# Kernel tuning notes

Measured on AMD Instinct MI355X. Metric: run time of the kernel, lower is better.

The kernel has to match this reference:

```python
import jax, jax.numpy as jnp
import numpy as np

B, S, D, E, K = 4, 2048, 1024, 8, 2
EPS, W_THRES, TEMP = 1e-4, 0.1, 1.0


def setup_inputs() -> dict:
    key = jax.random.key(0)
    k1, k2, k3, k4, k5 = jax.random.split(key, 5)
    x = jax.random.normal(k1, (B, S, D), dtype=jnp.float32)
    gate_W = jax.random.normal(k2, (D, E), dtype=jnp.float32) * 0.02
    gate_b = jnp.zeros((E,), dtype=jnp.float32)
    expert_W = jax.random.normal(k3, (E, D, D), dtype=jnp.float32) * 0.02
    expert_b = jnp.zeros((E, D), dtype=jnp.float32)
    return {"x": x, "gate_W": gate_W, "gate_b": gate_b,
            "expert_W": expert_W, "expert_b": expert_b}


def reference(x, gate_W, gate_b, expert_W, expert_b):
    # Gating: linear -> temperature -> clamp-min(eps) -> softmax
    scores = jnp.maximum((x @ gate_W + gate_b) / TEMP, EPS)      # [B,S,E]
    p = jax.nn.softmax(scores, axis=-1)                           # [B,S,E]
    _, topk_idx = jax.lax.top_k(p, K)                             # [B,S,K]
    # boolean membership mask of selected experts
    topk_mask = jax.nn.one_hot(topk_idx, E, dtype=p.dtype).sum(-2) > 0  # [B,S,E]
    # weights: clamp-min(weight_thres), normalized by detached sum over selected
    w = jnp.maximum(p, W_THRES)                                   # [B,S,E]
    w_gather = jnp.take_along_axis(w, topk_idx, axis=-1)          # [B,S,K]
    total = jax.lax.stop_gradient(w_gather.sum(-1, keepdims=True))
    w = w / total
    comb = jnp.where(topk_mask, w, jnp.zeros_like(w))             # [B,S,E]
    # Dense equivalent of gather/expert/scatter loop (E small): each expert
    # is Linear(D, D); masked combine weights zero out unselected experts.
    y = jnp.einsum('bsd,edf->bsef', x, expert_W) + expert_b       # [B,S,E,D]
    out = jnp.einsum('bsef,bse->bsf', y, comb) / K                # [B,S,D]
    return out
```

## Files before the change

kernel.cpp:

```cpp
#include <hip/hip_runtime.h>
#include <hip/hip_fp16.h>
#include <stdint.h>

#define TOK 8192
#define DIM 1024
#define NE 8
#define NTILE 136

typedef short bf16x8 __attribute__((ext_vector_type(8)));
typedef float f32x4 __attribute__((ext_vector_type(4)));

__device__ __forceinline__ unsigned short f2bf(float f) {
  unsigned int u = __float_as_uint(f);
  u += 0x7FFFu + ((u >> 16) & 1u);
  return (unsigned short)(u >> 16);
}

__device__ __forceinline__ void gl_lds16(const void* g, void* l) {
  __builtin_amdgcn_global_load_lds(
      (__attribute__((address_space(1))) unsigned int*)(g),
      (__attribute__((address_space(3))) unsigned int*)(l), 16, 0, 0);
}

__global__ __launch_bounds__(256) void gate_kernel(
    const float* __restrict__ x, const float* __restrict__ gW,
    const float* __restrict__ gb, unsigned short* __restrict__ xb,
    int* __restrict__ eSel, float* __restrict__ wSel, int* __restrict__ cnt)
{
  if (blockIdx.x == 0 && threadIdx.x < NE) cnt[threadIdx.x] = 0;

  __shared__ float gWs[NE * DIM];
#pragma unroll
  for (int h = 0; h < 8; ++h) {
    const int m = threadIdx.x + h * 256;
    float4 v = ((const float4*)gW)[m];
    const int d = m >> 1, e0 = (m & 1) * 4;
    gWs[(e0 + 0) * DIM + d] = v.x;
    gWs[(e0 + 1) * DIM + d] = v.y;
    gWs[(e0 + 2) * DIM + d] = v.z;
    gWs[(e0 + 3) * DIM + d] = v.w;
  }
  __syncthreads();

  const int wave = threadIdx.x >> 6;
  const int lane = threadIdx.x & 63;
  const int t = blockIdx.x * 4 + wave;
  const float4* xrow = (const float4*)(x + (size_t)t * DIM);
  ushort4* xbrow = (ushort4*)(xb + (size_t)t * DIM);

  double acc[NE];
#pragma unroll
  for (int e = 0; e < NE; ++e) acc[e] = 0.0;

#pragma unroll
  for (int i = 0; i < 4; ++i) {
    const int j = i * 64 + lane;
    float4 v = xrow[j];
    ushort4 pk;
    pk.x = f2bf(v.x); pk.y = f2bf(v.y); pk.z = f2bf(v.z); pk.w = f2bf(v.w);
    xbrow[j] = pk;
#pragma unroll
    for (int e = 0; e < NE; ++e) {
      float4 gv = *(const float4*)&gWs[e * DIM + j * 4];
      acc[e] += (double)v.x * (double)gv.x + (double)v.y * (double)gv.y
              + (double)v.z * (double)gv.z + (double)v.w * (double)gv.w;
    }
  }
#pragma unroll
  for (int off = 32; off > 0; off >>= 1) {
#pragma unroll
    for (int e = 0; e < NE; ++e)
      acc[e] += __shfl_xor(acc[e], off, 64);
  }

  if (lane == 0) {
    double s[NE];
#pragma unroll
    for (int e = 0; e < NE; ++e) {
      s[e] = acc[e] + (double)gb[e];
      if (s[e] < 1e-4) s[e] = 1e-4;
    }
    int e0 = 0;
    for (int e = 1; e < NE; ++e) if (s[e] > s[e0]) e0 = e;
    int e1 = (e0 == 0) ? 1 : 0;
    for (int e = 0; e < NE; ++e) if (e != e0 && s[e] > s[e1]) e1 = e;
    float m = (float)s[e0];
    float Z = 0.f, pf[NE];
#pragma unroll
    for (int e = 0; e < NE; ++e) { pf[e] = __expf((float)s[e] - m); Z += pf[e]; }
    float w0 = pf[e0] / Z; if (w0 < 0.1f) w0 = 0.1f;
    float w1 = pf[e1] / Z; if (w1 < 0.1f) w1 = 0.1f;
    const float inv = 0.5f / (w0 + w1);
    eSel[t * 2 + 0] = e0;
    eSel[t * 2 + 1] = e1;
    wSel[t * 2 + 0] = w0 * inv;
    wSel[t * 2 + 1] = w1 * inv;
  }
}

__global__ __launch_bounds__(256) void scatter_kernel(
    const int* __restrict__ eSel, const float* __restrict__ wSel,
    int* __restrict__ cnt, int* __restrict__ listTok, float* __restrict__ listW)
{
  __shared__ int lcnt[NE];
  __shared__ int base[NE];
  const int tid = threadIdx.x;
  if (tid < NE) lcnt[tid] = 0;
  __syncthreads();

  const int t = blockIdx.x * 256 + tid;
  const int e0 = eSel[t * 2 + 0];
  const int e1 = eSel[t * 2 + 1];
  const float w0 = wSel[t * 2 + 0];
  const float w1 = wSel[t * 2 + 1];
  const int l0 = atomicAdd(&lcnt[e0], 1);
  const int l1 = atomicAdd(&lcnt[e1], 1);
  __syncthreads();
  if (tid < NE) base[tid] = atomicAdd(&cnt[tid], lcnt[tid]);
  __syncthreads();

  const int p0 = base[e0] + l0;
  listTok[e0 * TOK + p0] = t * 2 + 0;
  listW [e0 * TOK + p0] = w0;
  const int p1 = base[e1] + l1;
  listTok[e1 * TOK + p1] = t * 2 + 1;
  listW [e1 * TOK + p1] = w1;
}

__global__ __launch_bounds__(256) void transpose_w(
    const float* __restrict__ W, unsigned short* __restrict__ Wt)
{
  __shared__ float t2[64][65];
  const int b  = blockIdx.x;
  const int e  = b >> 8;
  const int db = (b >> 4) & 15;
  const int fb = b & 15;
  const int d0 = db * 64, f0 = fb * 64;
  const int tid = threadIdx.x;
#pragma unroll
  for (int h = 0; h < 4; ++h) {
    const int idx = tid + h * 256;
    const int r = idx >> 4, c4 = idx & 15;
    float4 v = *(const float4*)&W[((size_t)e * DIM + d0 + r) * DIM + f0 + c4 * 4];
    t2[r][c4 * 4 + 0] = v.x;
    t2[r][c4 * 4 + 1] = v.y;
    t2[r][c4 * 4 + 2] = v.z;
    t2[r][c4 * 4 + 3] = v.w;
  }
  __syncthreads();
#pragma unroll
  for (int h = 0; h < 8; ++h) {
    const int o = tid + h * 256;
    const int f = o >> 5, k2 = (o & 31) * 2;
    const unsigned int lo = f2bf(t2[k2][f]);
    const unsigned int hi = f2bf(t2[k2 + 1][f]);
    *(unsigned int*)&Wt[((size_t)e * DIM + f0 + f) * DIM + d0 + k2] =
        lo | (hi << 16);
  }
}

__global__ __launch_bounds__(256) void moe_gemm(
    const unsigned short* __restrict__ xb, const unsigned short* __restrict__ Wt,
    const float* __restrict__ eb, const int* __restrict__ cnt,
    const int* __restrict__ listTok, const float* __restrict__ listW,
    __half* __restrict__ yslot)
{
  const int dId = blockIdx.x % NTILE;
  const int cT  = blockIdx.x / NTILE;
  int e = -1, r0 = 0, rows = 0, accT = 0;
#pragma unroll
  for (int ee = 0; ee < NE; ++ee) {
    const int c = cnt[ee];
    const int nt = (c + 127) >> 7;
    if (dId >= accT && dId < accT + nt) {
      e = ee; r0 = (dId - accT) * 128;
      rows = c - r0; if (rows > 128) rows = 128;
    }
    accT += nt;
  }
  if (e < 0) return;

  __shared__ __align__(16) unsigned short As[4][128 * 32];
  __shared__ __align__(16) unsigned short Bs[4][128 * 32];
  __shared__ int   tid_s[128];
  __shared__ float w_s[128];

  const int tid = threadIdx.x;
  if (tid < 128) {
    if (tid < rows) {
      tid_s[tid] = listTok[e * TOK + r0 + tid];
      w_s[tid]   = listW [e * TOK + r0 + tid];
    } else {
      tid_s[tid] = 0;
      w_s[tid]   = 0.0f;
    }
  }
  __syncthreads();

  const int w    = tid >> 6;
  const int lane = tid & 63;
  const int qsrc = (lane & 3) ^ ((lane >> 3) & 3);
  const int rA0  = w * 32 + (lane >> 2);
  const int rA1  = rA0 + 16;
  const unsigned short* srcA0 = xb + (size_t)(tid_s[rA0] >> 1) * DIM + qsrc * 8;
  const unsigned short* srcA1 = xb + (size_t)(tid_s[rA1] >> 1) * DIM + qsrc * 8;
  const unsigned short* srcB0 = Wt + ((size_t)e * DIM + cT * 128 + rA0) * DIM + qsrc * 8;
  const unsigned short* srcB1 = Wt + ((size_t)e * DIM + cT * 128 + rA1) * DIM + qsrc * 8;

  const int wr = w >> 1, wc = w & 1;
  const int mrow = lane & 15;
  const int qg   = lane >> 4;
  const int qsA  = (qg ^ ((mrow >> 1) & 3)) * 8;

  f32x4 acc[4][4];
#pragma unroll
  for (int i = 0; i < 4; ++i)
#pragma unroll
    for (int j = 0; j < 4; ++j)
      acc[i][j] = {0.f, 0.f, 0.f, 0.f};

#pragma unroll
  for (int p = 0; p < 3; ++p) {
    unsigned short* a = &As[p][w * 1024];
    unsigned short* b = &Bs[p][w * 1024];
    gl_lds16(srcA0 + p * 32, a);
    gl_lds16(srcA1 + p * 32, a + 512);
    gl_lds16(srcB0 + p * 32, b);
    gl_lds16(srcB1 + p * 32, b + 512);
  }
  asm volatile("s_waitcnt vmcnt(8)" ::: "memory");
  __builtin_amdgcn_s_barrier();

  for (int kc = 0; kc < DIM / 32; ++kc) {
    const int cur = kc & 3;
    if (kc + 3 < DIM / 32) {
      const int k1 = (kc + 3) * 32;
      const int nb = (kc + 3) & 3;
      unsigned short* a = &As[nb][w * 1024];
      unsigned short* b = &Bs[nb][w * 1024];
      gl_lds16(srcA0 + k1, a);
      gl_lds16(srcA1 + k1, a + 512);
      gl_lds16(srcB0 + k1, b);
      gl_lds16(srcB1 + k1, b + 512);
    }
    bf16x8 af[4], bfr[4];
#pragma unroll
    for (int mt = 0; mt < 4; ++mt)
      af[mt] = *(const bf16x8*)&As[cur][(wr * 64 + mt * 16 + mrow) * 32 + qsA];
#pragma unroll
    for (int nt = 0; nt < 4; ++nt)
      bfr[nt] = *(const bf16x8*)&Bs[cur][(wc * 64 + nt * 16 + mrow) * 32 + qsA];
#pragma unroll
    for (int mt = 0; mt < 4; ++mt)
#pragma unroll
      for (int nt = 0; nt < 4; ++nt)
        acc[mt][nt] = __builtin_amdgcn_mfma_f32_16x16x32_bf16(
            af[mt], bfr[nt], acc[mt][nt], 0, 0, 0);
    if (kc < DIM / 32 - 1) {
      if (kc < DIM / 32 - 3)
        asm volatile("s_waitcnt vmcnt(8) lgkmcnt(0)" ::: "memory");
      else if (kc == DIM / 32 - 3)
        asm volatile("s_waitcnt vmcnt(4) lgkmcnt(0)" ::: "memory");
      else
        asm volatile("s_waitcnt vmcnt(0) lgkmcnt(0)" ::: "memory");
      __builtin_amdgcn_s_barrier();
    }
  }

  const int colBase = cT * 128 + wc * 64 + mrow;
  float bias[4];
#pragma unroll
  for (int nt = 0; nt < 4; ++nt)
    bias[nt] = eb[(size_t)e * DIM + colBase + nt * 16];
#pragma unroll
  for (int mt = 0; mt < 4; ++mt) {
#pragma unroll
    for (int r = 0; r < 4; ++r) {
      const int rloc = wr * 64 + mt * 16 + (lane >> 4) * 4 + r;
      if (rloc < rows) {
        const int tk    = tid_s[rloc];
        const float wgt = w_s[rloc];
        __half* dst = yslot + ((size_t)(tk & 1) * TOK + (size_t)(tk >> 1)) * DIM;
#pragma unroll
        for (int nt = 0; nt < 4; ++nt)
          dst[colBase + nt * 16] = __float2half(wgt * (acc[mt][nt][r] + bias[nt]));
      }
    }
  }
}

__global__ __launch_bounds__(256) void combine(
    const __half* __restrict__ y0, const __half* __restrict__ y1,
    float4* __restrict__ out)
{
  const size_t i = (size_t)blockIdx.x * 256 + threadIdx.x;
  const ushort4 ua = ((const ushort4*)y0)[i];
  const ushort4 ub = ((const ushort4*)y1)[i];
  const __half* ah = (const __half*)&ua;
  const __half* bh = (const __half*)&ub;
  float4 o;
  o.x = __half2float(ah[0]) + __half2float(bh[0]);
  o.y = __half2float(ah[1]) + __half2float(bh[1]);
  o.z = __half2float(ah[2]) + __half2float(bh[2]);
  o.w = __half2float(ah[3]) + __half2float(bh[3]);
  out[i] = o;
}

extern "C" void kernel_launch(void* const* d_in, const int* in_sizes, int n_in,
                              void* d_out, int out_size, void* d_ws, size_t ws_size,
                              hipStream_t stream)
{
  const float* x  = (const float*)d_in[0];
  const float* gW = (const float*)d_in[1];
  const float* gb = (const float*)d_in[2];
  const float* eW = (const float*)d_in[3];
  const float* eb = (const float*)d_in[4];
  float* out = (float*)d_out;

  char* p = (char*)d_ws;
  unsigned short* xb = (unsigned short*)p;  p += (size_t)TOK * DIM * 2;
  unsigned short* Wt = (unsigned short*)p;  p += (size_t)NE * DIM * DIM * 2;
  __half* yslot = (__half*)p;               p += (size_t)2 * TOK * DIM * 2;
  int* cnt = (int*)p;                       p += 256;
  int* listTok = (int*)p;                   p += (size_t)NE * TOK * 4;
  float* listW = (float*)p;                 p += (size_t)NE * TOK * 4;

  int*   eSel = (int*)yslot;
  float* wSel = (float*)((char*)yslot + TOK * 8);

  gate_kernel<<<TOK / 4, 256, 0, stream>>>(x, gW, gb, xb, eSel, wSel, cnt);
  scatter_kernel<<<TOK / 256, 256, 0, stream>>>(eSel, wSel, cnt, listTok, listW);
  transpose_w<<<NE * 256, 256, 0, stream>>>(eW, Wt);
  moe_gemm<<<NTILE * 8, 256, 0, stream>>>(xb, Wt, eb, cnt, listTok, listW, yslot);
  combine<<<TOK * DIM / 4 / 256, 256, 0, stream>>>(
      yslot, yslot + (size_t)TOK * DIM, (float4*)out);
}
```

Measured before the change: 214.1 us.

## Widen MoE GEMM tile to 128x256 with 512 threads and phased pipeline

The expert GEMM block goes from 256 threads computing a 128x128 tile to 512 threads computing a 128x256 tile. The grid drops from 8 to 4 column tiles per row tile, and each token row of A is loaded once per 256 output columns, halving A re-reads. The K loop is restructured into half-chunk phases with a 3-stage LDS ring, a barrier between LDS reads and MFMA, and s_setprio raised around the MFMA block, with an explicit vmcnt wait schedule. This raises LDS use and halves the number of blocks, which risks lower occupancy and less parallelism for the small-expert tiles.

Result: faster. 208.3 us (-2.7%).

```diff
diff --git a/kernel.cpp b/kernel.cpp
--- a/kernel.cpp
+++ b/kernel.cpp
@@ -6,6 +6,7 @@
 #define DIM 1024
 #define NE 8
 #define NTILE 136
+#define NCT 4
 
 typedef short bf16x8 __attribute__((ext_vector_type(8)));
 typedef float f32x4 __attribute__((ext_vector_type(4)));
@@ -159,7 +160,40 @@
   }
 }
 
-__global__ __launch_bounds__(256) void moe_gemm(
+#define WAITVM(n) asm volatile("s_waitcnt vmcnt(" #n ")" ::: "memory")
+
+#define STG3(t, h, stb)                                                      \
+  { const int off_ = (t) * 64 + (h) * 32;                                    \
+    unsigned short* Ad_ = (unsigned short*)As + ((stb) * 2 + (h)) * (128 * 32) + w * 512;  \
+    unsigned short* Bd_ = (unsigned short*)Bs + ((stb) * 2 + (h)) * (256 * 32) + w * 1024; \
+    gl_lds16(srcA  + off_, Ad_);                                             \
+    gl_lds16(srcB0 + off_, Bd_);                                             \
+    gl_lds16(srcB1 + off_, Bd_ + 512); }
+
+#define PHASE(t, h, bufv, stb, DO_STAGE, VMA)                                \
+  { const unsigned short* Ab_ = (const unsigned short*)As + ((bufv) * 2 + (h)) * (128 * 32); \
+    const unsigned short* Bb_ = (const unsigned short*)Bs + ((bufv) * 2 + (h)) * (256 * 32); \
+    bf16x8 af[4], bfr[4];                                                    \
+    _Pragma("unroll")                                                        \
+    for (int mt = 0; mt < 4; ++mt)                                           \
+      af[mt] = *(const bf16x8*)&Ab_[(wr * 64 + mt * 16 + mrow) * 32 + sA];   \
+    _Pragma("unroll")                                                        \
+    for (int nt = 0; nt < 4; ++nt)                                           \
+      bfr[nt] = *(const bf16x8*)&Bb_[(wc * 64 + nt * 16 + mrow) * 32 + sA];  \
+    if (DO_STAGE) { STG3((t) + 2, h, stb); }                                 \
+    __builtin_amdgcn_s_barrier();                                            \
+    __builtin_amdgcn_s_setprio(1);                                           \
+    _Pragma("unroll")                                                        \
+    for (int mt = 0; mt < 4; ++mt)                                           \
+      _Pragma("unroll")                                                      \
+      for (int nt = 0; nt < 4; ++nt)                                         \
+        acc[mt][nt] = __builtin_amdgcn_mfma_f32_16x16x32_bf16(               \
+            af[mt], bfr[nt], acc[mt][nt], 0, 0, 0);                          \
+    __builtin_amdgcn_s_setprio(0);                                           \
+    VMA;                                                                     \
+    __builtin_amdgcn_s_barrier(); }
+
+__global__ __launch_bounds__(512, 2) void moe_gemm(
     const unsigned short* __restrict__ xb, const unsigned short* __restrict__ Wt,
     const float* __restrict__ eb, const int* __restrict__ cnt,
     const int* __restrict__ listTok, const float* __restrict__ listW,
@@ -180,8 +214,8 @@
   }
   if (e < 0) return;
 
-  __shared__ __align__(16) unsigned short As[4][128 * 32];
-  __shared__ __align__(16) unsigned short Bs[4][128 * 32];
+  __shared__ __align__(16) unsigned short As[3 * 2 * 128 * 32];
+  __shared__ __align__(16) unsigned short Bs[3 * 2 * 256 * 32];
   __shared__ int   tid_s[128];
   __shared__ float w_s[128];
 
@@ -199,18 +233,19 @@
 
   const int w    = tid >> 6;
   const int lane = tid & 63;
-  const int qsrc = (lane & 3) ^ ((lane >> 3) & 3);
-  const int rA0  = w * 32 + (lane >> 2);
-  const int rA1  = rA0 + 16;
-  const unsigned short* srcA0 = xb + (size_t)(tid_s[rA0] >> 1) * DIM + qsrc * 8;
-  const unsigned short* srcA1 = xb + (size_t)(tid_s[rA1] >> 1) * DIM + qsrc * 8;
-  const unsigned short* srcB0 = Wt + ((size_t)e * DIM + cT * 128 + rA0) * DIM + qsrc * 8;
-  const unsigned short* srcB1 = Wt + ((size_t)e * DIM + cT * 128 + rA1) * DIM + qsrc * 8;
-
-  const int wr = w >> 1, wc = w & 1;
+  const int rA  = w * 16 + (lane >> 2);
+  const int qA  = (lane & 3) ^ (rA & 3);
+  const unsigned short* srcA = xb + (size_t)(tid_s[rA] >> 1) * DIM + qA * 8;
+  const int rB0 = w * 32 + (lane >> 2);
+  const int rB1 = rB0 + 16;
+  const int qB  = (lane & 3) ^ (rB0 & 3);
+  const unsigned short* srcB0 = Wt + ((size_t)e * DIM + cT * 256 + rB0) * DIM + qB * 8;
+  const unsigned short* srcB1 = Wt + ((size_t)e * DIM + cT * 256 + rB1) * DIM + qB * 8;
+
+  const int wr = w >> 2, wc = w & 3;
   const int mrow = lane & 15;
   const int qg   = lane >> 4;
-  const int qsA  = (qg ^ ((mrow >> 1) & 3)) * 8;
+  const int sA   = (qg ^ (mrow & 3)) * 8;
 
   f32x4 acc[4][4];
 #pragma unroll
@@ -219,55 +254,24 @@
     for (int j = 0; j < 4; ++j)
       acc[i][j] = {0.f, 0.f, 0.f, 0.f};
 
-#pragma unroll
-  for (int p = 0; p < 3; ++p) {
-    unsigned short* a = &As[p][w * 1024];
-    unsigned short* b = &Bs[p][w * 1024];
-    gl_lds16(srcA0 + p * 32, a);
-    gl_lds16(srcA1 + p * 32, a + 512);
-    gl_lds16(srcB0 + p * 32, b);
-    gl_lds16(srcB1 + p * 32, b + 512);
-  }
-  asm volatile("s_waitcnt vmcnt(8)" ::: "memory");
+  STG3(0, 0, 0); STG3(0, 1, 0); STG3(1, 0, 1); STG3(1, 1, 1);
+  WAITVM(9);
   __builtin_amdgcn_s_barrier();
 
-  for (int kc = 0; kc < DIM / 32; ++kc) {
-    const int cur = kc & 3;
-    if (kc + 3 < DIM / 32) {
-      const int k1 = (kc + 3) * 32;
-      const int nb = (kc + 3) & 3;
-      unsigned short* a = &As[nb][w * 1024];
-      unsigned short* b = &Bs[nb][w * 1024];
-      gl_lds16(srcA0 + k1, a);
-      gl_lds16(srcA1 + k1, a + 512);
-      gl_lds16(srcB0 + k1, b);
-      gl_lds16(srcB1 + k1, b + 512);
-    }
-    bf16x8 af[4], bfr[4];
-#pragma unroll
-    for (int mt = 0; mt < 4; ++mt)
-      af[mt] = *(const bf16x8*)&As[cur][(wr * 64 + mt * 16 + mrow) * 32 + qsA];
-#pragma unroll
-    for (int nt = 0; nt < 4; ++nt)
-      bfr[nt] = *(const bf16x8*)&Bs[cur][(wc * 64 + nt * 16 + mrow) * 32 + qsA];
-#pragma unroll
-    for (int mt = 0; mt < 4; ++mt)
-#pragma unroll
-      for (int nt = 0; nt < 4; ++nt)
-        acc[mt][nt] = __builtin_amdgcn_mfma_f32_16x16x32_bf16(
-            af[mt], bfr[nt], acc[mt][nt], 0, 0, 0);
-    if (kc < DIM / 32 - 1) {
-      if (kc < DIM / 32 - 3)
-        asm volatile("s_waitcnt vmcnt(8) lgkmcnt(0)" ::: "memory");
-      else if (kc == DIM / 32 - 3)
-        asm volatile("s_waitcnt vmcnt(4) lgkmcnt(0)" ::: "memory");
-      else
-        asm volatile("s_waitcnt vmcnt(0) lgkmcnt(0)" ::: "memory");
-      __builtin_amdgcn_s_barrier();
-    }
-  }
-
-  const int colBase = cT * 128 + wc * 64 + mrow;
+  int buf = 0, stb = 2;
+#pragma unroll 1
+  for (int t = 0; t < 14; ++t) {
+    PHASE(t, 0, buf, stb, true, WAITVM(9));
+    PHASE(t, 1, buf, stb, true, WAITVM(9));
+    buf = (buf == 2) ? 0 : buf + 1;
+    stb = (stb == 2) ? 0 : stb + 1;
+  }
+  PHASE(14, 0, 2, 0, false, WAITVM(6));
+  PHASE(14, 1, 2, 0, false, WAITVM(3));
+  PHASE(15, 0, 0, 0, false, WAITVM(0));
+  PHASE(15, 1, 0, 0, false, ((void)0));
+
+  const int colBase = cT * 256 + wc * 64 + mrow;
   float bias[4];
 #pragma unroll
   for (int nt = 0; nt < 4; ++nt)
@@ -331,7 +335,7 @@
   gate_kernel<<<TOK / 4, 256, 0, stream>>>(x, gW, gb, xb, eSel, wSel, cnt);
   scatter_kernel<<<TOK / 256, 256, 0, stream>>>(eSel, wSel, cnt, listTok, listW);
   transpose_w<<<NE * 256, 256, 0, stream>>>(eW, Wt);
-  moe_gemm<<<NTILE * 8, 256, 0, stream>>>(xb, Wt, eb, cnt, listTok, listW, yslot);
+  moe_gemm<<<NTILE * NCT, 512, 0, stream>>>(xb, Wt, eb, cnt, listTok, listW, yslot);
   combine<<<TOK * DIM / 4 / 256, 256, 0, stream>>>(
       yslot, yslot + (size_t)TOK * DIM, (float4*)out);
 }
```
